# Performance work log

Measured on AMD Instinct MI355X. Metric: run time of the kernel, lower is better.

Reference implementation:

```python
import jax, jax.numpy as jnp
import numpy as np

N = 50_000          # nodes
E = 1_600_000       # edges (avg degree 32)
IN = 128            # in_feats
H = 4               # num_heads
F = 32              # out_feats per head
CUTOFF = 4.0        # bessel_cutoff
P = 7               # envelope_exponent + 1
ENV_A = -(P + 1) * (P + 2) / 2.0   # -36
ENV_B = P * (P + 2)                # 63
ENV_C = -P * (P + 1) / 2.0         # -28


def setup_inputs() -> dict:
    key = jax.random.key(0)
    ks = jax.random.split(key, 8)
    x = jax.random.normal(ks[0], (N, IN), dtype=jnp.float32)
    distance = jax.random.uniform(ks[1], (E,), dtype=jnp.float32) * CUTOFF
    W_src = jax.random.normal(ks[2], (H * F, IN), dtype=jnp.float32) * 0.05
    b_src = jnp.zeros((H * F,), dtype=jnp.float32)
    W_dst = jax.random.normal(ks[3], (H * F, IN), dtype=jnp.float32) * 0.05
    b_dst = jnp.zeros((H * F,), dtype=jnp.float32)
    attn = jax.random.normal(ks[4], (1, H, F), dtype=jnp.float32) * 0.1
    prelu_alpha = jnp.full((H,), 0.25, dtype=jnp.float32)
    frequencies = jnp.arange(1.0, H + 1.0, dtype=jnp.float32) * np.pi
    src = jax.random.randint(ks[5], (E,), 0, N, dtype=jnp.int32)
    dst = jax.random.randint(ks[6], (E,), 0, N, dtype=jnp.int32)
    return dict(x=x, distance=distance, W_src=W_src, b_src=b_src,
                W_dst=W_dst, b_dst=b_dst, attn=attn,
                prelu_alpha=prelu_alpha, frequencies=frequencies,
                src=src, dst=dst)


def _bessel_coeff(distance, frequencies):
    # distance: [E] -> d_scaled: [E,1]; frequencies: [H] -> coeff: [E,H]
    d = (distance / CUTOFF)[:, None]
    d_p0 = d ** P
    env = d + ENV_A * d_p0 + ENV_B * (d_p0 * d) + ENV_C * (d_p0 * d * d)
    return env * jnp.sin(frequencies * d)


def reference(x, distance, W_src, b_src, W_dst, b_dst, attn,
              prelu_alpha, frequencies, src, dst):
    n = x.shape[0]
    feat_src = (x @ W_src.T + b_src).reshape(n, H, F)   # [N,H,F]
    feat_dst = (x @ W_dst.T + b_dst).reshape(n, H, F)   # [N,H,F]

    coeff = _bessel_coeff(distance, frequencies)[:, :, None]  # [E,H,1]

    el = feat_src[src]                                  # [E,H,F] gather
    e = (el + feat_dst[dst]) * coeff                    # u_add_v then bessel scale
    e = jnp.where(e >= 0, e, prelu_alpha[None, :, None] * e)  # PReLU per head
    score = jnp.einsum('ehf,hf->eh', e, attn[0])        # [E,H]

    # edge softmax over incoming edges per dst node, per head
    seg_max = jax.ops.segment_max(score, dst, num_segments=n)        # [N,H]
    ex = jnp.exp(score - seg_max[dst])                               # [E,H]
    denom = jax.ops.segment_sum(ex, dst, num_segments=n)             # [N,H]
    a = ex / denom[dst]                                              # [E,H]

    # u_mul_e + scatter-sum aggregation
    msgs = el * a[:, :, None]                                        # [E,H,F]
    rst = jax.ops.segment_sum(msgs, dst, num_segments=n)             # [N,H,F]
    return rst
```

## Files before the change

### kernel.cpp

```cpp
#include <hip/hip_runtime.h>
#include <hip/hip_bf16.h>
#include <math.h>

#define N_NODES 50000
#define E_EDGES 1600000
#define HF 128
#define INV_CUTOFF 0.25f
#define ENV_A -36.0f
#define ENV_B 63.0f
#define ENV_C -28.0f

#define GEMM_BLOCKS ((N_NODES + 63) / 64)
#define REC_CAP 72
#define NBUCK 196
#define BUCK_CAP 8960
#define EPB 6250

typedef __attribute__((ext_vector_type(8))) short bf16x8;
typedef __attribute__((ext_vector_type(4))) float f32x4;

__device__ __forceinline__ unsigned short f2bf(float f) {
  unsigned u = __float_as_uint(f);
  u += 0x7fffu + ((u >> 16) & 1u);
  return (unsigned short)(u >> 16);
}
__device__ __forceinline__ unsigned pack2(float lo, float hi) {
  return (unsigned)f2bf(lo) | ((unsigned)f2bf(hi) << 16);
}
__device__ __forceinline__ float2 up2(unsigned v) {
  return make_float2(__uint_as_float(v << 16), __uint_as_float(v & 0xffff0000u));
}
__device__ __forceinline__ float2 pk_fma(float2 a, float2 b, float2 c) {
  return make_float2(fmaf(a.x, b.x, c.x), fmaf(a.y, b.y, c.y));
}
__device__ __forceinline__ float2 pk_add(float2 a, float2 b) {
  return make_float2(a.x + b.x, a.y + b.y);
}
__device__ __forceinline__ float2 pk_max0(float2 a) {
  return make_float2(fmaxf(a.x, 0.f), fmaxf(a.y, 0.f));
}
__device__ __forceinline__ float2 pk_min0(float2 a) {
  return make_float2(fminf(a.x, 0.f), fminf(a.y, 0.f));
}

__global__ void prep_w(const float* __restrict__ Ws, const float* __restrict__ Wd,
                       unsigned short* __restrict__ wbf) {
  const int q = blockIdx.x * 256 + threadIdx.x;
  if (q < 4096) {
    const int n = q >> 4, c = q & 15;
    const float* Wp = ((n < 128) ? Ws : Wd) + (size_t)(n & 127) * HF + c * 8;
    const float4 v0 = *(const float4*)Wp;
    const float4 v1 = *(const float4*)(Wp + 4);
    uint4 pk;
    pk.x = pack2(v0.x, v0.y); pk.y = pack2(v0.z, v0.w);
    pk.z = pack2(v1.x, v1.y); pk.w = pack2(v1.z, v1.w);
    *(uint4*)(wbf + (size_t)n * HF + ((c ^ (n & 15)) * 8)) = pk;
  }
}

__global__ __launch_bounds__(256) void feat_gemm(
    const float* __restrict__ x, const unsigned short* __restrict__ wbf,
    const float* __restrict__ bs, const float* __restrict__ bd,
    unsigned short* __restrict__ fs, float* __restrict__ fd) {
  __shared__ unsigned short wlds[256 * 128];

  for (int i = threadIdx.x; i < 4096; i += 256)
    ((uint4*)wlds)[i] = ((const uint4*)wbf)[i];

  const int lane = threadIdx.x & 63;
  const int wave = threadIdx.x >> 6;
  const int m = lane & 15;
  const int quad = lane >> 4;
  const int m0 = blockIdx.x * 64 + wave * 16;
  const int row = m0 + m;
  const int rowc = (row < N_NODES) ? row : (N_NODES - 1);

  union { bf16x8 v; unsigned u[4]; } af[4];
  #pragma unroll
  for (int kt = 0; kt < 4; kt++) {
    const float* xp = x + (size_t)rowc * HF + kt * 32 + quad * 8;
    const float4 u0 = *(const float4*)xp;
    const float4 u1 = *(const float4*)(xp + 4);
    af[kt].u[0] = pack2(u0.x, u0.y); af[kt].u[1] = pack2(u0.z, u0.w);
    af[kt].u[2] = pack2(u1.x, u1.y); af[kt].u[3] = pack2(u1.z, u1.w);
  }

  __syncthreads();

  float accA[16][4];
  #pragma unroll
  for (int nt = 0; nt < 16; nt++) {
    const int nrow = nt * 16 + m;
    f32x4 acc = {0.f, 0.f, 0.f, 0.f};
    #pragma unroll
    for (int kt = 0; kt < 4; kt++) {
      const int pc = (kt * 4 + quad) ^ m;
      const bf16x8 bf = *(const bf16x8*)(wlds + (size_t)nrow * HF + pc * 8);
      acc = __builtin_amdgcn_mfma_f32_16x16x32_bf16(af[kt].v, bf, acc, 0, 0, 0);
    }
    accA[nt][0] = acc[0]; accA[nt][1] = acc[1];
    accA[nt][2] = acc[2]; accA[nt][3] = acc[3];
  }

  __syncthreads();
  unsigned short* fsS = wlds;
  float* fdS = (float*)(wlds + 64 * 136);

  const int rl0 = wave * 16 + quad * 4;
  #pragma unroll
  for (int nt = 0; nt < 16; nt++) {
    const int col = nt * 16 + m;
    if (col < 128) {
      const float bias = bs[col];
      #pragma unroll
      for (int r = 0; r < 4; r++)
        fsS[(rl0 + r) * 136 + col] = f2bf(accA[nt][r] + bias);
    } else {
      const float bias = bd[col - 128];
      #pragma unroll
      for (int r = 0; r < 4; r++)
        fdS[(rl0 + r) * 132 + (col - 128)] = accA[nt][r] + bias;
    }
  }
  __syncthreads();

  for (int c = threadIdx.x; c < 1024; c += 256) {
    const int r = c >> 4, off = (c & 15) * 8;
    const int gr = blockIdx.x * 64 + r;
    if (gr < N_NODES)
      *(uint4*)(fs + (size_t)gr * HF + off) = *(const uint4*)(fsS + r * 136 + off);
  }
  for (int c = threadIdx.x; c < 2048; c += 256) {
    const int r = c >> 5, off = (c & 31) * 4;
    const int gr = blockIdx.x * 64 + r;
    if (gr < N_NODES)
      *(float4*)(fd + (size_t)gr * HF + off) = *(const float4*)(fdS + r * 132 + off);
  }
}

__global__ __launch_bounds__(256) void bucketize(
    const int* __restrict__ dst, const int* __restrict__ src,
    const float* __restrict__ dist,
    int* __restrict__ bcursor, unsigned* __restrict__ bb_pay,
    unsigned char* __restrict__ bb_loc) {
  __shared__ unsigned pay_s[EPB];
  __shared__ unsigned char bkt_s[EPB];
  __shared__ unsigned char loc_s[EPB];
  __shared__ int hist[NBUCK], loff[NBUCK], base[NBUCK], cur[NBUCK];
  for (int t = threadIdx.x; t < NBUCK; t += 256) { hist[t] = 0; cur[t] = 0; }
  __syncthreads();
  const int lo = blockIdx.x * EPB;
  for (int k = threadIdx.x; k < EPB; k += 256)
    atomicAdd(&hist[dst[lo + k] >> 8], 1);
  __syncthreads();
  if (threadIdx.x == 0) {
    int run = 0;
    for (int j = 0; j < NBUCK; j++) { loff[j] = run; run += hist[j]; }
  }
  __syncthreads();
  for (int t = threadIdx.x; t < NBUCK; t += 256)
    base[t] = atomicAdd(&bcursor[t], hist[t]);
  __syncthreads();
  for (int k = threadIdx.x; k < EPB; k += 256) {
    const int d = dst[lo + k];
    const int b = d >> 8;
    float ds = dist[lo + k] * (INV_CUTOFF * 65536.f);
    unsigned dq = (unsigned)(ds + 0.5f);
    if (dq > 65535u) dq = 65535u;
    const int s = loff[b] + atomicAdd(&cur[b], 1);
    pay_s[s] = (unsigned)src[lo + k] | (dq << 16);
    bkt_s[s] = (unsigned char)b;
    loc_s[s] = (unsigned char)(d & 255);
  }
  __syncthreads();
  for (int s = threadIdx.x; s < EPB; s += 256) {
    const int b = bkt_s[s];
    const int dest = base[b] + (s - loff[b]);
    if (dest < BUCK_CAP) {
      bb_pay[(size_t)b * BUCK_CAP + dest] = pay_s[s];
      bb_loc[(size_t)b * BUCK_CAP + dest] = loc_s[s];
    }
  }
}

__global__ __launch_bounds__(256) void bucket_scatter(
    const int* __restrict__ bcursor, const unsigned* __restrict__ bb_pay,
    const unsigned char* __restrict__ bb_loc,
    int* __restrict__ counts, unsigned* __restrict__ rec) {
  __shared__ int cnt[256];
  __shared__ unsigned recS[256 * REC_CAP];
  cnt[threadIdx.x] = 0;
  __syncthreads();
  const int b = blockIdx.x;
  const int total = min(bcursor[b], BUCK_CAP);
  const size_t base = (size_t)b * BUCK_CAP;
  for (int i = threadIdx.x; i < total; i += 256) {
    const unsigned pay = bb_pay[base + i];
    const int local = bb_loc[base + i];
    const int r = atomicAdd(&cnt[local], 1);
    if (r < REC_CAP) recS[local * REC_CAP + r] = pay;
  }
  __syncthreads();
  const int node0 = b << 8;
  uint4* dstp = (uint4*)(rec + (size_t)node0 * REC_CAP);
  const uint4* srcp = (const uint4*)recS;
  for (int i = threadIdx.x; i < 256 * REC_CAP / 4; i += 256)
    dstp[i] = srcp[i];
  const int node = node0 + (int)threadIdx.x;
  if (node < N_NODES) counts[node] = min(cnt[threadIdx.x], REC_CAP);
}

__global__ __launch_bounds__(256) void gat_agg(
    const unsigned short* __restrict__ fs, const float* __restrict__ fd,
    const int* __restrict__ counts, const unsigned* __restrict__ rec,
    const float* __restrict__ attn, const float* __restrict__ alpha_p,
    const float* __restrict__ freqs, float* __restrict__ out) {
  const int wave = threadIdx.x >> 6;
  const int lane = threadIdx.x & 63;
  const int node = blockIdx.x * 4 + wave;
  if (node >= N_NODES) return;
  const int eslot = lane >> 4;
  const int h = (lane >> 2) & 3;
  const int j = lane & 3;
  const int fo = (h << 5) + (j << 3);

  const float* fdp = fd + (size_t)node * HF + fo;
  const float2 f0 = *(const float2*)(fdp + 0);
  const float2 f1 = *(const float2*)(fdp + 2);
  const float2 f2 = *(const float2*)(fdp + 4);
  const float2 f3 = *(const float2*)(fdp + 6);
  const float2 t0 = *(const float2*)(attn + fo + 0);
  const float2 t1 = *(const float2*)(attn + fo + 2);
  const float2 t2 = *(const float2*)(attn + fo + 4);
  const float2 t3 = *(const float2*)(attn + fo + 6);
  const float al = alpha_p[h];
  const float fr = freqs[h];

  const int beg = node * REC_CAP;
  int cnt = counts[node];
  cnt = (cnt < REC_CAP) ? cnt : REC_CAP;
  const int end = beg + cnt;

  float l = 0.f;
  float2 A0 = {0.f, 0.f}, A1 = {0.f, 0.f}, A2 = {0.f, 0.f}, A3 = {0.f, 0.f};

  for (int i = beg; i < end; i += 4) {
    const int e = i + eslot;
    const bool valid = (e < end);
    const unsigned r = rec[valid ? e : beg];
    const int s_idx = (int)(r & 0xffffu);
    const float d = (float)(r >> 16) * (1.0f / 65536.0f);
    const uint4 eb = *(const uint4*)(fs + (size_t)s_idx * HF + fo);
    const float2 e0 = up2(eb.x);
    const float2 e1 = up2(eb.y);
    const float2 e2 = up2(eb.z);
    const float2 e3 = up2(eb.w);

    const float d2 = d * d;
    const float d4 = d2 * d2;
    const float d7 = d4 * d2 * d;
    const float env = fmaf(d7, fmaf(d, fmaf(d, ENV_C, ENV_B), ENV_A), d);
    const float cf = env * __sinf(fr * d);
    const float acf = al * cf;
    const float cpos = (cf >= 0.f) ? cf : acf;
    const float cneg = (cf >= 0.f) ? acf : cf;

    float2 sp = {0.f, 0.f}, sn = {0.f, 0.f};
    float2 u;
    u = pk_add(e0, f0); sp = pk_fma(pk_max0(u), t0, sp); sn = pk_fma(pk_min0(u), t0, sn);
    u = pk_add(e1, f1); sp = pk_fma(pk_max0(u), t1, sp); sn = pk_fma(pk_min0(u), t1, sn);
    u = pk_add(e2, f2); sp = pk_fma(pk_max0(u), t2, sp); sn = pk_fma(pk_min0(u), t2, sn);
    u = pk_add(e3, f3); sp = pk_fma(pk_max0(u), t3, sp); sn = pk_fma(pk_min0(u), t3, sn);
    float p = fmaf(cpos, sp.x + sp.y, cneg * (sn.x + sn.y));

    p += __shfl_xor(p, 1);
    p += __shfl_xor(p, 2);

    const float w = valid ? __expf(p) : 0.f;
    l += w;
    const float2 w2 = {w, w};
    A0 = pk_fma(w2, e0, A0);
    A1 = pk_fma(w2, e1, A1);
    A2 = pk_fma(w2, e2, A2);
    A3 = pk_fma(w2, e3, A3);
  }

  #pragma unroll
  for (int mm = 16; mm < 64; mm <<= 1) {
    l    += __shfl_xor(l, mm);
    A0.x += __shfl_xor(A0.x, mm); A0.y += __shfl_xor(A0.y, mm);
    A1.x += __shfl_xor(A1.x, mm); A1.y += __shfl_xor(A1.y, mm);
    A2.x += __shfl_xor(A2.x, mm); A2.y += __shfl_xor(A2.y, mm);
    A3.x += __shfl_xor(A3.x, mm); A3.y += __shfl_xor(A3.y, mm);
  }

  if (eslot == 0) {
    const float rl = (l > 0.f) ? 1.0f / l : 0.f;
    float* o = out + (size_t)node * HF + fo;
    float4 o0 = {A0.x * rl, A0.y * rl, A1.x * rl, A1.y * rl};
    float4 o1 = {A2.x * rl, A2.y * rl, A3.x * rl, A3.y * rl};
    *(float4*)o = o0;
    *(float4*)(o + 4) = o1;
  }
}

extern "C" void kernel_launch(void* const* d_in, const int* in_sizes, int n_in,
                              void* d_out, int out_size, void* d_ws, size_t ws_size,
                              hipStream_t stream) {
  const float* x      = (const float*)d_in[0];
  const float* dist   = (const float*)d_in[1];
  const float* W_src  = (const float*)d_in[2];
  const float* b_src  = (const float*)d_in[3];
  const float* W_dst  = (const float*)d_in[4];
  const float* b_dst  = (const float*)d_in[5];
  const float* attn   = (const float*)d_in[6];
  const float* alpha  = (const float*)d_in[7];
  const float* freqs  = (const float*)d_in[8];
  const int*   src    = (const int*)d_in[9];
  const int*   dst    = (const int*)d_in[10];
  float* out = (float*)d_out;

  char* w = (char*)d_ws;
  size_t off = 0;
  auto alloc = [&](size_t bytes) -> void* {
    void* p = w + off;
    off += (bytes + 255) & ~(size_t)255;
    return p;
  };
  unsigned short* feat_src = (unsigned short*)alloc((size_t)N_NODES * HF * 2);
  float*          feat_dst = (float*)alloc((size_t)N_NODES * HF * 4);
  unsigned short* wbf      = (unsigned short*)alloc((size_t)256 * HF * 2);
  int*            counts   = (int*)alloc((size_t)N_NODES * 4);
  int*            bcursor  = (int*)alloc((size_t)NBUCK * 4);
  unsigned*       bb_pay   = (unsigned*)alloc((size_t)NBUCK * BUCK_CAP * 4);
  unsigned char*  bb_loc   = (unsigned char*)alloc((size_t)NBUCK * BUCK_CAP);
  unsigned*       rec      = (unsigned*)alloc((size_t)NBUCK * 256 * REC_CAP * 4);

  hipMemsetAsync(bcursor, 0, (size_t)NBUCK * 4, stream);

  prep_w<<<16, 256, 0, stream>>>(W_src, W_dst, wbf);

  feat_gemm<<<GEMM_BLOCKS, 256, 0, stream>>>(x, wbf, b_src, b_dst, feat_src, feat_dst);

  bucketize<<<256, 256, 0, stream>>>(dst, src, dist, bcursor, bb_pay, bb_loc);

  bucket_scatter<<<NBUCK, 256, 0, stream>>>(bcursor, bb_pay, bb_loc, counts, rec);

  gat_agg<<<(N_NODES + 3) / 4, 256, 0, stream>>>(
      feat_src, feat_dst, counts, rec, attn, alpha, freqs, out);
}
```

Measured before the change: 253.0 us.

## Split bucket scatter across blocks, prefetch gathers, and simplify PReLU scoring

Each destination bucket is now processed by four blocks, each holding a smaller shared staging area. Per-node records are appended to the global list through atomic counters, which requires zeroing the counts array beforehand. The aggregation kernel software-pipelines the record and feature-row loads one step ahead and exits early for nodes with no incoming edges. It also rewrites the PReLU dot product as a linear term plus an absolute-value term, issued through inline packed-f32 instructions. The gain is more parallelism and less shared memory in the scatter stage and fewer instructions in the hot loop, at the cost of global atomics and a nondeterministic record order.

```diff
diff --git a/kernel.cpp b/kernel.cpp
--- a/kernel.cpp
+++ b/kernel.cpp
@@ -15,6 +15,8 @@
 #define NBUCK 196
 #define BUCK_CAP 8960
 #define EPB 6250
+#define SPLIT 4
+#define LCAP 32
 
 typedef __attribute__((ext_vector_type(8))) short bf16x8;
 typedef __attribute__((ext_vector_type(4))) float f32x4;
@@ -30,17 +32,22 @@
 __device__ __forceinline__ float2 up2(unsigned v) {
   return make_float2(__uint_as_float(v << 16), __uint_as_float(v & 0xffff0000u));
 }
+
+__device__ __forceinline__ float2 pk_add(float2 a, float2 b) {
+  float2 d;
+  asm("v_pk_add_f32 %0, %1, %2" : "=v"(d) : "v"(a), "v"(b));
+  return d;
+}
 __device__ __forceinline__ float2 pk_fma(float2 a, float2 b, float2 c) {
-  return make_float2(fmaf(a.x, b.x, c.x), fmaf(a.y, b.y, c.y));
-}
-__device__ __forceinline__ float2 pk_add(float2 a, float2 b) {
-  return make_float2(a.x + b.x, a.y + b.y);
-}
-__device__ __forceinline__ float2 pk_max0(float2 a) {
-  return make_float2(fmaxf(a.x, 0.f), fmaxf(a.y, 0.f));
-}
-__device__ __forceinline__ float2 pk_min0(float2 a) {
-  return make_float2(fminf(a.x, 0.f), fminf(a.y, 0.f));
+  float2 d;
+  asm("v_pk_fma_f32 %0, %1, %2, %3" : "=v"(d) : "v"(a), "v"(b), "v"(c));
+  return d;
+}
+__device__ __forceinline__ float2 pk_abs(float2 a) {
+  float2 d;
+  d.x = __uint_as_float(__float_as_uint(a.x) & 0x7fffffffu);
+  d.y = __uint_as_float(__float_as_uint(a.y) & 0x7fffffffu);
+  return d;
 }
 
 __global__ void prep_w(const float* __restrict__ Ws, const float* __restrict__ Wd,
@@ -188,26 +195,35 @@
     const unsigned char* __restrict__ bb_loc,
     int* __restrict__ counts, unsigned* __restrict__ rec) {
   __shared__ int cnt[256];
-  __shared__ unsigned recS[256 * REC_CAP];
+  __shared__ unsigned recS[256 * LCAP];
   cnt[threadIdx.x] = 0;
   __syncthreads();
-  const int b = blockIdx.x;
+  const int b = blockIdx.x / SPLIT;
+  const int q = blockIdx.x - b * SPLIT;
   const int total = min(bcursor[b], BUCK_CAP);
+  const int lo = (total * q) / SPLIT;
+  const int hi = (total * (q + 1)) / SPLIT;
   const size_t base = (size_t)b * BUCK_CAP;
-  for (int i = threadIdx.x; i < total; i += 256) {
+  for (int i = lo + threadIdx.x; i < hi; i += 256) {
     const unsigned pay = bb_pay[base + i];
     const int local = bb_loc[base + i];
     const int r = atomicAdd(&cnt[local], 1);
-    if (r < REC_CAP) recS[local * REC_CAP + r] = pay;
-  }
-  __syncthreads();
-  const int node0 = b << 8;
-  uint4* dstp = (uint4*)(rec + (size_t)node0 * REC_CAP);
-  const uint4* srcp = (const uint4*)recS;
-  for (int i = threadIdx.x; i < 256 * REC_CAP / 4; i += 256)
-    dstp[i] = srcp[i];
-  const int node = node0 + (int)threadIdx.x;
-  if (node < N_NODES) counts[node] = min(cnt[threadIdx.x], REC_CAP);
+    if (r < LCAP) recS[local * LCAP + r] = pay;
+  }
+  __syncthreads();
+  const int node = (b << 8) + (int)threadIdx.x;
+  if (node < N_NODES) {
+    const int cl = min(cnt[threadIdx.x], LCAP);
+    if (cl > 0) {
+      const int gbase = atomicAdd(&counts[node], cl);
+      unsigned* dstp = rec + (size_t)node * REC_CAP;
+      const unsigned* srcp = recS + threadIdx.x * LCAP;
+      for (int k = 0; k < cl; k++) {
+        const int pos = gbase + k;
+        if (pos < REC_CAP) dstp[pos] = srcp[k];
+      }
+    }
+  }
 }
 
 __global__ __launch_bounds__(256) void gat_agg(
@@ -224,6 +240,19 @@
   const int j = lane & 3;
   const int fo = (h << 5) + (j << 3);
 
+  int cnt = counts[node];
+  cnt = (cnt < REC_CAP) ? cnt : REC_CAP;
+
+  if (cnt <= 0) {
+    if (eslot == 0) {
+      float* o = out + (size_t)node * HF + fo;
+      float4 z = {0.f, 0.f, 0.f, 0.f};
+      *(float4*)o = z;
+      *(float4*)(o + 4) = z;
+    }
+    return;
+  }
+
   const float* fdp = fd + (size_t)node * HF + fo;
   const float2 f0 = *(const float2*)(fdp + 0);
   const float2 f1 = *(const float2*)(fdp + 2);
@@ -234,23 +263,34 @@
   const float2 t2 = *(const float2*)(attn + fo + 4);
   const float2 t3 = *(const float2*)(attn + fo + 6);
   const float al = alpha_p[h];
+  const float c1 = 0.5f * (1.0f + al);
+  const float c2 = 0.5f * (1.0f - al);
   const float fr = freqs[h];
 
   const int beg = node * REC_CAP;
-  int cnt = counts[node];
-  cnt = (cnt < REC_CAP) ? cnt : REC_CAP;
   const int end = beg + cnt;
+  const int last = end - 1;
+  const unsigned short* fsp = fs + fo;
+
+  int e0i = beg + eslot;
+  unsigned rcur = rec[(e0i < end) ? e0i : last];
+  uint4 ebcur = *(const uint4*)(fsp + ((size_t)(rcur & 0xffffu) << 7));
+  int e1i = beg + 4 + eslot;
+  unsigned rnext = rec[(e1i < end) ? e1i : last];
 
   float l = 0.f;
   float2 A0 = {0.f, 0.f}, A1 = {0.f, 0.f}, A2 = {0.f, 0.f}, A3 = {0.f, 0.f};
 
   for (int i = beg; i < end; i += 4) {
-    const int e = i + eslot;
-    const bool valid = (e < end);
-    const unsigned r = rec[valid ? e : beg];
-    const int s_idx = (int)(r & 0xffffu);
+    const unsigned r = rcur;
+    const uint4 eb = ebcur;
+    rcur = rnext;
+    const int inn = i + 8 + eslot;
+    rnext = rec[(inn < end) ? inn : last];
+    ebcur = *(const uint4*)(fsp + ((size_t)(rcur & 0xffffu) << 7));
+
+    const bool valid = (i + eslot < end);
     const float d = (float)(r >> 16) * (1.0f / 65536.0f);
-    const uint4 eb = *(const uint4*)(fs + (size_t)s_idx * HF + fo);
     const float2 e0 = up2(eb.x);
     const float2 e1 = up2(eb.y);
     const float2 e2 = up2(eb.z);
@@ -261,18 +301,17 @@
     const float d7 = d4 * d2 * d;
     const float env = fmaf(d7, fmaf(d, fmaf(d, ENV_C, ENV_B), ENV_A), d);
     const float cf = env * __sinf(fr * d);
-    const float acf = al * cf;
-    const float cpos = (cf >= 0.f) ? cf : acf;
-    const float cneg = (cf >= 0.f) ? acf : cf;
-
-    float2 sp = {0.f, 0.f}, sn = {0.f, 0.f};
+    const float k1 = c1 * cf;
+    const float k2 = c2 * fabsf(cf);
+
+    float2 D1 = {0.f, 0.f}, D2 = {0.f, 0.f};
     float2 u;
-    u = pk_add(e0, f0); sp = pk_fma(pk_max0(u), t0, sp); sn = pk_fma(pk_min0(u), t0, sn);
-    u = pk_add(e1, f1); sp = pk_fma(pk_max0(u), t1, sp); sn = pk_fma(pk_min0(u), t1, sn);
-    u = pk_add(e2, f2); sp = pk_fma(pk_max0(u), t2, sp); sn = pk_fma(pk_min0(u), t2, sn);
-    u = pk_add(e3, f3); sp = pk_fma(pk_max0(u), t3, sp); sn = pk_fma(pk_min0(u), t3, sn);
-    float p = fmaf(cpos, sp.x + sp.y, cneg * (sn.x + sn.y));
-
+    u = pk_add(e0, f0); D1 = pk_fma(u, t0, D1); D2 = pk_fma(pk_abs(u), t0, D2);
+    u = pk_add(e1, f1); D1 = pk_fma(u, t1, D1); D2 = pk_fma(pk_abs(u), t1, D2);
+    u = pk_add(e2, f2); D1 = pk_fma(u, t2, D1); D2 = pk_fma(pk_abs(u), t2, D2);
+    u = pk_add(e3, f3); D1 = pk_fma(u, t3, D1); D2 = pk_fma(pk_abs(u), t3, D2);
+
+    float p = fmaf(k1, D1.x + D1.y, k2 * (D2.x + D2.y));
     p += __shfl_xor(p, 1);
     p += __shfl_xor(p, 2);
 
@@ -337,6 +376,7 @@
   unsigned*       rec      = (unsigned*)alloc((size_t)NBUCK * 256 * REC_CAP * 4);
 
   hipMemsetAsync(bcursor, 0, (size_t)NBUCK * 4, stream);
+  hipMemsetAsync(counts, 0, (size_t)N_NODES * 4, stream);
 
   prep_w<<<16, 256, 0, stream>>>(W_src, W_dst, wbf);
 
@@ -344,7 +384,7 @@
 
   bucketize<<<256, 256, 0, stream>>>(dst, src, dist, bcursor, bb_pay, bb_loc);
 
-  bucket_scatter<<<NBUCK, 256, 0, stream>>>(bcursor, bb_pay, bb_loc, counts, rec);
+  bucket_scatter<<<NBUCK * SPLIT, 256, 0, stream>>>(bcursor, bb_pay, bb_loc, counts, rec);
 
   gat_agg<<<(N_NODES + 3) / 4, 256, 0, stream>>>(
       feat_src, feat_dst, counts, rec, attn, alpha, freqs, out);
```

Measured after the change: 253.0 us. No clear change (+0.0%).
